# Kernel optimization log

Measured on AMD Instinct MI355X. Metric: run time of the kernel, lower is better.

## Reference

```python
import jax, jax.numpy as jnp
import numpy as np

B, N = 64, 4096          # trees per batch, leaves per complete binary tree
V, S = 21, 50            # amino-acid vocab, grammar-symbol vocab
E, H = 64, 128           # embed_dim, hidden_dim


def setup_inputs() -> dict:
    key = jax.random.key(0)
    ks = jax.random.split(key, 16)

    def lin_w(k, din, dout):
        return (jax.random.normal(k, (dout, din), jnp.float32) / np.sqrt(din)).astype(jnp.float32)

    tokens = jax.random.randint(ks[0], (B, N), 0, V, dtype=jnp.int32)
    symbols = jax.random.randint(ks[1], (B, N - 1), 0, S, dtype=jnp.int32)

    emb = jax.random.normal(ks[2], (V, E), jnp.float32) * 0.02
    emb = emb.at[0].set(0.0)  # padding_idx=0
    sym_emb = jax.random.normal(ks[3], (S, E), jnp.float32) * 0.02

    return {
        "tokens": tokens, "symbols": symbols,
        "emb": emb, "sym_emb": sym_emb,
        "Wp": lin_w(ks[4], E, H), "bp": jnp.zeros((H,), jnp.float32),
        "Wi": lin_w(ks[5], H, H), "bi": jnp.zeros((H,), jnp.float32),
        "Ui": lin_w(ks[6], H, H),
        "Wf": lin_w(ks[7], H, H), "bf": jnp.zeros((H,), jnp.float32),
        "Uf": lin_w(ks[8], H, H),
        "Wo": lin_w(ks[9], H, H), "bo": jnp.zeros((H,), jnp.float32),
        "Uo": lin_w(ks[10], H, H),
        "Wu": lin_w(ks[11], H, H), "bu": jnp.zeros((H,), jnp.float32),
        "Uu": lin_w(ks[12], H, H),
        "Wout": lin_w(ks[13], H, H), "bout": jnp.zeros((H,), jnp.float32),
    }


def _encode(tokens, symbols, emb, sym_emb, Wp, bp, Wi, bi, Ui, Wf, bf, Uf,
            Wo, bo, Uo, Wu, bu, Uu, Wout, bout):
    emb = emb.at[0].set(0.0)  # padding row contributes nothing (and gets no grad)

    # Leaf nodes: amino-acid embedding -> input_proj, no children.
    x = emb[tokens] @ Wp.T + bp                      # [B, N, H]
    i = jax.nn.sigmoid(x @ Wi.T + bi)
    o = jax.nn.sigmoid(x @ Wo.T + bo)
    u = jnp.tanh(x @ Wu.T + bu)
    c = i * u                                        # [B, N, H]
    h = o * jnp.tanh(c)

    # Bottom-up over levels of the complete binary tree (Child-Sum Tree-LSTM).
    off, n = 0, N
    while n > 1:
        m = n // 2
        xs = sym_emb[symbols[:, off:off + m]] @ Wp.T + bp   # [B, m, H]
        hl, hr = h[:, 0::2], h[:, 1::2]
        cl, cr = c[:, 0::2], c[:, 1::2]
        ht = hl + hr                                         # h_tilde = sum_j h_j
        gi = jax.nn.sigmoid(xs @ Wi.T + bi + ht @ Ui.T)
        go = jax.nn.sigmoid(xs @ Wo.T + bo + ht @ Uo.T)
        gu = jnp.tanh(xs @ Wu.T + bu + ht @ Uu.T)
        fx = xs @ Wf.T + bf
        fl = jax.nn.sigmoid(fx + hl @ Uf.T)                  # per-child forget gates
        fr = jax.nn.sigmoid(fx + hr @ Uf.T)
        c = gi * gu + fl * cl + fr * cr
        h = go * jnp.tanh(c)
        off += m
        n = m

    root_h = h[:, 0]                                         # [B, H]
    return root_h @ Wout.T + bout                            # output_proj


def reference(tokens, symbols, emb, sym_emb, Wp, bp, Wi, bi, Ui, Wf, bf, Uf,
              Wo, bo, Uo, Wu, bu, Uu, Wout, bout):
    return _encode(tokens, symbols, emb, sym_emb, Wp, bp, Wi, bi, Ui, Wf, bf,
                   Uf, Wo, bo, Uo, Wu, bu, Uu, Wout, bout)
```

## Files before the change

kernel.cpp:

```cpp
#include <hip/hip_runtime.h>
#include <hip/hip_bf16.h>

typedef __attribute__((ext_vector_type(8))) short short8;
typedef __attribute__((ext_vector_type(4))) float f32x4;

static constexpr int B_ = 64;
static constexpr int N_ = 4096;
static constexpr int V_ = 21;
static constexpr int S_ = 50;
static constexpr int E_ = 64;
static constexpr int H_ = 128;
static constexpr int NPAIR = V_ * V_;
static constexpr int NTAB = NPAIR * S_;

__device__ __forceinline__ float rcp_(float x) { return __builtin_amdgcn_rcpf(x); }
__device__ __forceinline__ float sigm(float x) { return rcp_(1.0f + __expf(-x)); }
__device__ __forceinline__ float tanh_(float x) {
  float a = fabsf(x);
  float e = __expf(-2.0f * a);
  float t = (1.0f - e) * rcp_(1.0f + e);
  return x < 0.0f ? -t : t;
}
__device__ __forceinline__ unsigned short f2bf(float f) {
  __hip_bfloat16 b = __float2bfloat16(f);
  return *reinterpret_cast<unsigned short*>(&b);
}
__device__ __forceinline__ float bf2f(unsigned short u) {
  return __uint_as_float(((unsigned int)u) << 16);
}

struct Gates { float cv, hv; };
__device__ __forceinline__ Gates gate_combine(const float* __restrict__ sx, int cc,
    float i_p, float o_p, float u_p, float fl_p, float fr_p, float cl, float cr) {
  float gi = sigm(sx[cc] + i_p);
  float go = sigm(sx[128 + cc] + o_p);
  float gu = tanh_(sx[256 + cc] + u_p);
  float fx = sx[384 + cc];
  float fl = sigm(fx + fl_p);
  float fr = sigm(fx + fr_p);
  float cv = fmaf(gi, gu, fmaf(fl, cl, fr * cr));
  Gates g; g.cv = cv; g.hv = go * tanh_(cv);
  return g;
}

__global__ void k_pre0(const float* __restrict__ Ui, const float* __restrict__ Uo,
                       const float* __restrict__ Uu, const float* __restrict__ Uf,
                       const float* __restrict__ Wi, const float* __restrict__ Wo,
                       const float* __restrict__ Wu, const float* __restrict__ Wf,
                       const float* __restrict__ Wp,
                       unsigned short* __restrict__ Wfrag, float* __restrict__ Wt,
                       float* __restrict__ Wxt, float* __restrict__ Wpt) {
  int blk = blockIdx.x, t = threadIdx.x;
  if (blk < 32) {
    int idx = blk * 256 + t;
    int L = idx & 63;
    int K = (idx >> 6) & 3;
    int T = idx >> 8;
    int n = 16 * T + (L & 15);
    int k0 = 32 * K + ((L >> 4) << 3);
    int g = n >> 7, o = n & 127;
    const float* U = (g == 0) ? Ui : (g == 1) ? Uo : (g == 2) ? Uu : Uf;
    unsigned short out[8];
    #pragma unroll
    for (int j = 0; j < 8; ++j) out[j] = f2bf(U[o * 128 + k0 + j]);
    *(int4*)(Wfrag + (size_t)idx * 8) = *(int4*)out;
  } else if (blk < 96) {
    bool isU = blk < 64;
    int base = (((blk & 31)) * 256 + t) * 8;
    int k = base >> 9;
    int col = base & 511;
    int gg = col >> 7, o0 = col & 127;
    const float* M;
    if (isU) M = (gg == 0) ? Ui : (gg == 1) ? Uo : (gg == 2) ? Uu : Uf;
    else     M = (gg == 0) ? Wi : (gg == 1) ? Wo : (gg == 2) ? Wu : Wf;
    float* D = isU ? Wt : Wxt;
    float v[8];
    #pragma unroll
    for (int j = 0; j < 8; ++j) v[j] = M[(o0 + j) * 128 + k];
    *(float4*)(D + base) = *(float4*)v;
    *(float4*)(D + base + 4) = *(float4*)(v + 4);
  } else {
    for (int i = t; i < E_ * H_; i += 256) {
      int e = i >> 7, o = i & 127;
      Wpt[i] = Wp[o * E_ + e];
    }
  }
}

__global__ void k_pre1(const float* __restrict__ emb, const float* __restrict__ sym_emb,
                       const float* __restrict__ Wpt, const float* __restrict__ Wxt,
                       const float* __restrict__ bp, const float* __restrict__ bi,
                       const float* __restrict__ bo, const float* __restrict__ bu,
                       const float* __restrict__ bfv,
                       unsigned short* __restrict__ leaf_h8, float* __restrict__ leaf_c,
                       float* __restrict__ symx) {
  int blk = blockIdx.x, t = threadIdx.x;
  __shared__ float x[128];
  if (blk < V_) {
    int v = blk;
    float acc = bp[t];
    if (v != 0) {
      for (int e = 0; e < E_; ++e) acc = fmaf(emb[v * E_ + e], Wpt[e * 128 + t], acc);
    }
    x[t] = acc;
    __syncthreads();
    float zi = bi[t], zo = bo[t], zu = bu[t];
    for (int k = 0; k < H_; ++k) {
      float xv = x[k];
      const float* wr = Wxt + k * 512;
      zi = fmaf(xv, wr[t], zi);
      zo = fmaf(xv, wr[128 + t], zo);
      zu = fmaf(xv, wr[256 + t], zu);
    }
    float gi = sigm(zi), go = sigm(zo), gu = tanh_(zu);
    float c = gi * gu;
    leaf_c[v * H_ + t] = c;
    leaf_h8[v * H_ + t] = f2bf(go * tanh_(c));
  } else {
    int s = blk - V_;
    float acc = bp[t];
    for (int e = 0; e < E_; ++e) acc = fmaf(sym_emb[s * E_ + e], Wpt[e * 128 + t], acc);
    x[t] = acc;
    __syncthreads();
    float zi = bi[t], zo = bo[t], zu = bu[t], zf = bfv[t];
    for (int k = 0; k < H_; ++k) {
      float xv = x[k];
      const float* wr = Wxt + k * 512;
      zi = fmaf(xv, wr[t], zi);
      zo = fmaf(xv, wr[128 + t], zo);
      zu = fmaf(xv, wr[256 + t], zu);
      zf = fmaf(xv, wr[384 + t], zf);
    }
    size_t base = (size_t)s * 4 * H_;
    symx[base + 0 * H_ + t] = zi;
    symx[base + 1 * H_ + t] = zo;
    symx[base + 2 * H_ + t] = zu;
    symx[base + 3 * H_ + t] = zf;
  }
}

__global__ void k_tabA(const unsigned short* __restrict__ leaf_h8, const float* __restrict__ Wt,
                       float* __restrict__ za) {
  int p = blockIdx.x, t = threadIdx.x;
  int tl = p / V_, tr = p % V_;
  __shared__ float hl[128], hr[128];
  hl[t] = bf2f(leaf_h8[tl * H_ + t]);
  hr[t] = bf2f(leaf_h8[tr * H_ + t]);
  __syncthreads();
  float zi = 0.f, zo = 0.f, zu = 0.f, pfl = 0.f, pfr = 0.f;
  for (int k = 0; k < H_; ++k) {
    float l = hl[k], r = hr[k], ht = l + r;
    const float* wr = Wt + k * 512;
    zi = fmaf(ht, wr[t], zi);
    zo = fmaf(ht, wr[128 + t], zo);
    zu = fmaf(ht, wr[256 + t], zu);
    float wf = wr[384 + t];
    pfl = fmaf(l, wf, pfl);
    pfr = fmaf(r, wf, pfr);
  }
  float* z = za + (size_t)p * 640;
  z[t] = zi; z[128 + t] = zo; z[256 + t] = zu; z[384 + t] = pfl; z[512 + t] = pfr;
}

__global__ void k_tabB(const float* __restrict__ za, const float* __restrict__ symx,
                       const float* __restrict__ leaf_c,
                       const int* __restrict__ tokens, const int* __restrict__ symbols,
                       unsigned short* __restrict__ tab_h8, float* __restrict__ tab_c,
                       int* __restrict__ idx1) {
  int blk = blockIdx.x, t = threadIdx.x;
  if (blk < NTAB / 2) {
    int row = blk * 2 + (t >> 7);
    int u = t & 127;
    int p = row / S_, s = row - p * S_;
    int tl = p / V_, tr = p - tl * V_;
    const float* z = za + (size_t)p * 640;
    const float* sx = symx + (size_t)s * 512;
    float gi = sigm(sx[u] + z[u]);
    float go = sigm(sx[128 + u] + z[128 + u]);
    float gu = tanh_(sx[256 + u] + z[256 + u]);
    float fx = sx[384 + u];
    float fl = sigm(fx + z[384 + u]);
    float fr = sigm(fx + z[512 + u]);
    float cv = fmaf(gi, gu, fmaf(fl, leaf_c[tl * H_ + u], fr * leaf_c[tr * H_ + u]));
    tab_c[(size_t)row * H_ + u] = cv;
    tab_h8[(size_t)row * H_ + u] = f2bf(go * tanh_(cv));
  } else {
    int g = (blk - NTAB / 2) * 256 + t;
    int b = g >> 11, j = g & 2047;
    idx1[g] = (tokens[b * N_ + 2 * j] * V_ + tokens[b * N_ + 2 * j + 1]) * S_ + symbols[b * (N_ - 1) + j];
  }
}

__global__ void __launch_bounds__(512, 4) k_lvl23(
    const unsigned short* __restrict__ Wfrag, const float* __restrict__ symx,
    const int* __restrict__ symbols, const int* __restrict__ idx1,
    const unsigned short* __restrict__ gh8, const float* __restrict__ gc,
    unsigned short* __restrict__ h_out8, float* __restrict__ c_out) {
  __shared__ __align__(16) unsigned short Ag[64][136];
  __shared__ __align__(16) unsigned short Bh[32][136];
  __shared__ float Bc[32][132];
  int t = threadIdx.x;
  int w = t >> 6, L = t & 63, q = L >> 4, cL = L & 15;
  int cc = 16 * w + cL;
  int g0 = blockIdx.x * 32;
  int b = g0 >> 10;
  int j2 = g0 & 1023;
  const int* sym_b = symbols + (size_t)b * (N_ - 1);
  const int* gix = idx1 + 2 * g0;

  #pragma unroll
  for (int i = 0; i < 2; ++i) {
    int fid = t + 512 * i;
    int row = fid >> 4, co = (fid & 15) * 8;
    *(int4*)&Ag[row][co] = *(const int4*)(gh8 + (size_t)gix[row] * H_ + co);
  }
  __syncthreads();

  const short8* wf = (const short8*)Wfrag;
  #pragma unroll
  for (int c = 0; c < 2; ++c) {
    f32x4 acc[2][4];
    #pragma unroll
    for (int r = 0; r < 2; ++r)
      #pragma unroll
      for (int g = 0; g < 4; ++g) acc[r][g] = (f32x4){0.f, 0.f, 0.f, 0.f};
    #pragma unroll
    for (int K = 0; K < 4; ++K) {
      short8 bfr[4];
      #pragma unroll
      for (int g = 0; g < 4; ++g) bfr[g] = wf[(size_t)((w + 8 * g) * 4 + K) * 64 + L];
      short8 a0 = *(const short8*)&Ag[32 * c + cL][K * 32 + q * 8];
      short8 a1 = *(const short8*)&Ag[32 * c + 16 + cL][K * 32 + q * 8];
      #pragma unroll
      for (int g = 0; g < 4; ++g) {
        acc[0][g] = __builtin_amdgcn_mfma_f32_16x16x32_bf16(a0, bfr[g], acc[0][g], 0, 0, 0);
        acc[1][g] = __builtin_amdgcn_mfma_f32_16x16x32_bf16(a1, bfr[g], acc[1][g], 0, 0, 0);
      }
    }
    #pragma unroll
    for (int r = 0; r < 2; ++r) {
      #pragma unroll
      for (int nd = 0; nd < 2; ++nd) {
        int n = 16 * c + 8 * r + 2 * q + nd;
        int s = sym_b[2048 + j2 + n];
        const float* sx = symx + (size_t)s * 512;
        float clv = gc[(size_t)gix[2 * n] * H_ + cc];
        float crv = gc[(size_t)gix[2 * n + 1] * H_ + cc];
        Gates gt = gate_combine(sx, cc,
            acc[r][0][2 * nd] + acc[r][0][2 * nd + 1],
            acc[r][1][2 * nd] + acc[r][1][2 * nd + 1],
            acc[r][2][2 * nd] + acc[r][2][2 * nd + 1],
            acc[r][3][2 * nd], acc[r][3][2 * nd + 1], clv, crv);
        Bc[n][cc] = gt.cv;
        Bh[n][cc] = f2bf(gt.hv);
      }
    }
  }
  __syncthreads();
  {
    f32x4 acc[2][4];
    #pragma unroll
    for (int r = 0; r < 2; ++r)
      #pragma unroll
      for (int g = 0; g < 4; ++g) acc[r][g] = (f32x4){0.f, 0.f, 0.f, 0.f};
    #pragma unroll
    for (int K = 0; K < 4; ++K) {
      short8 bfr[4];
      #pragma unroll
      for (int g = 0; g < 4; ++g) bfr[g] = wf[(size_t)((w + 8 * g) * 4 + K) * 64 + L];
      short8 a0 = *(const short8*)&Bh[cL][K * 32 + q * 8];
      short8 a1 = *(const short8*)&Bh[16 + cL][K * 32 + q * 8];
      #pragma unroll
      for (int g = 0; g < 4; ++g) {
        acc[0][g] = __builtin_amdgcn_mfma_f32_16x16x32_bf16(a0, bfr[g], acc[0][g], 0, 0, 0);
        acc[1][g] = __builtin_amdgcn_mfma_f32_16x16x32_bf16(a1, bfr[g], acc[1][g], 0, 0, 0);
      }
    }
    #pragma unroll
    for (int r = 0; r < 2; ++r) {
      #pragma unroll
      for (int nd = 0; nd < 2; ++nd) {
        int n = 8 * r + 2 * q + nd;
        int G3 = (g0 >> 1) + n;
        int s = sym_b[3072 + (j2 >> 1) + n];
        const float* sx = symx + (size_t)s * 512;
        Gates gt = gate_combine(sx, cc,
            acc[r][0][2 * nd] + acc[r][0][2 * nd + 1],
            acc[r][1][2 * nd] + acc[r][1][2 * nd + 1],
            acc[r][2][2 * nd] + acc[r][2][2 * nd + 1],
            acc[r][3][2 * nd], acc[r][3][2 * nd + 1],
            Bc[2 * n][cc], Bc[2 * n + 1][cc]);
        c_out[(size_t)G3 * H_ + cc] = gt.cv;
        h_out8[(size_t)G3 * H_ + cc] = f2bf(gt.hv);
      }
    }
  }
}

__global__ void __launch_bounds__(512, 4) k_lvl45(
    const unsigned short* __restrict__ Wfrag, const float* __restrict__ symx,
    const int* __restrict__ symbols,
    const unsigned short* __restrict__ in_h8, const float* __restrict__ in_c,
    unsigned short* __restrict__ h_out8, float* __restrict__ c_out) {
  __shared__ __align__(16) unsigned short Ag[64][136];
  __shared__ __align__(16) unsigned short Bh[32][136];
  __shared__ float Bc[32][132];
  int t = threadIdx.x;
  int w = t >> 6, L = t & 63, q = L >> 4, cL = L & 15;
  int cc = 16 * w + cL;
  int g0 = blockIdx.x * 32;
  int b = g0 >> 8;
  int j4 = g0 & 255;
  const int* sym_b = symbols + (size_t)b * (N_ - 1);

  #pragma unroll
  for (int i = 0; i < 2; ++i) {
    int fid = t + 512 * i;
    int row = fid >> 4, co = (fid & 15) * 8;
    *(int4*)&Ag[row][co] = *(const int4*)(in_h8 + (size_t)(2 * g0 + row) * H_ + co);
  }
  __syncthreads();

  const short8* wf = (const short8*)Wfrag;
  #pragma unroll
  for (int c = 0; c < 2; ++c) {
    f32x4 acc[2][4];
    #pragma unroll
    for (int r = 0; r < 2; ++r)
      #pragma unroll
      for (int g = 0; g < 4; ++g) acc[r][g] = (f32x4){0.f, 0.f, 0.f, 0.f};
    #pragma unroll
    for (int K = 0; K < 4; ++K) {
      short8 bfr[4];
      #pragma unroll
      for (int g = 0; g < 4; ++g) bfr[g] = wf[(size_t)((w + 8 * g) * 4 + K) * 64 + L];
      short8 a0 = *(const short8*)&Ag[32 * c + cL][K * 32 + q * 8];
      short8 a1 = *(const short8*)&Ag[32 * c + 16 + cL][K * 32 + q * 8];
      #pragma unroll
      for (int g = 0; g < 4; ++g) {
        acc[0][g] = __builtin_amdgcn_mfma_f32_16x16x32_bf16(a0, bfr[g], acc[0][g], 0, 0, 0);
        acc[1][g] = __builtin_amdgcn_mfma_f32_16x16x32_bf16(a1, bfr[g], acc[1][g], 0, 0, 0);
      }
    }
    #pragma unroll
    for (int r = 0; r < 2; ++r) {
      #pragma unroll
      for (int nd = 0; nd < 2; ++nd) {
        int n = 16 * c + 8 * r + 2 * q + nd;
        int g = g0 + n;
        int s = sym_b[3584 + j4 + n];
        const float* sx = symx + (size_t)s * 512;
        Gates gt = gate_combine(sx, cc,
            acc[r][0][2 * nd] + acc[r][0][2 * nd + 1],
            acc[r][1][2 * nd] + acc[r][1][2 * nd + 1],
            acc[r][2][2 * nd] + acc[r][2][2 * nd + 1],
            acc[r][3][2 * nd], acc[r][3][2 * nd + 1],
            in_c[(size_t)(2 * g) * H_ + cc], in_c[(size_t)(2 * g + 1) * H_ + cc]);
        Bc[n][cc] = gt.cv;
        Bh[n][cc] = f2bf(gt.hv);
      }
    }
  }
  __syncthreads();
  {
    f32x4 acc[2][4];
    #pragma unroll
    for (int r = 0; r < 2; ++r)
      #pragma unroll
      for (int g = 0; g < 4; ++g) acc[r][g] = (f32x4){0.f, 0.f, 0.f, 0.f};
    #pragma unroll
    for (int K = 0; K < 4; ++K) {
      short8 bfr[4];
      #pragma unroll
      for (int g = 0; g < 4; ++g) bfr[g] = wf[(size_t)((w + 8 * g) * 4 + K) * 64 + L];
      short8 a0 = *(const short8*)&Bh[cL][K * 32 + q * 8];
      short8 a1 = *(const short8*)&Bh[16 + cL][K * 32 + q * 8];
      #pragma unroll
      for (int g = 0; g < 4; ++g) {
        acc[0][g] = __builtin_amdgcn_mfma_f32_16x16x32_bf16(a0, bfr[g], acc[0][g], 0, 0, 0);
        acc[1][g] = __builtin_amdgcn_mfma_f32_16x16x32_bf16(a1, bfr[g], acc[1][g], 0, 0, 0);
      }
    }
    #pragma unroll
    for (int r = 0; r < 2; ++r) {
      #pragma unroll
      for (int nd = 0; nd < 2; ++nd) {
        int n = 8 * r + 2 * q + nd;
        int G5 = (g0 >> 1) + n;
        int s = sym_b[3840 + (j4 >> 1) + n];
        const float* sx = symx + (size_t)s * 512;
        Gates gt = gate_combine(sx, cc,
            acc[r][0][2 * nd] + acc[r][0][2 * nd + 1],
            acc[r][1][2 * nd] + acc[r][1][2 * nd + 1],
            acc[r][2][2 * nd] + acc[r][2][2 * nd + 1],
            acc[r][3][2 * nd], acc[r][3][2 * nd + 1],
            Bc[2 * n][cc], Bc[2 * n + 1][cc]);
        c_out[(size_t)G5 * H_ + cc] = gt.cv;
        h_out8[(size_t)G5 * H_ + cc] = f2bf(gt.hv);
      }
    }
  }
}

__global__ void __launch_bounds__(512, 2) k_lvl6(
    const unsigned short* __restrict__ Wfrag, const float* __restrict__ symx,
    const int* __restrict__ symbols,
    const unsigned short* __restrict__ h_prev8, const float* __restrict__ c_prev,
    unsigned short* __restrict__ h_out8, float* __restrict__ c_out) {
  __shared__ __align__(16) unsigned short Asm[32][136];
  int t = threadIdx.x;
  int w = t >> 6, L = t & 63, q = L >> 4, cL = L & 15;
  int g0 = blockIdx.x * 16;

  {
    int row = t >> 4, co = (t & 15) * 8;
    *(int4*)&Asm[row][co] = *(const int4*)(h_prev8 + (size_t)(2 * g0 + row) * H_ + co);
  }
  __syncthreads();

  f32x4 acc[2][4];
  #pragma unroll
  for (int r = 0; r < 2; ++r)
    #pragma unroll
    for (int g = 0; g < 4; ++g) acc[r][g] = (f32x4){0.f, 0.f, 0.f, 0.f};

  const short8* wf = (const short8*)Wfrag;
  #pragma unroll
  for (int K = 0; K < 4; ++K) {
    short8 bfr[4];
    #pragma unroll
    for (int g = 0; g < 4; ++g) bfr[g] = wf[(size_t)((w + 8 * g) * 4 + K) * 64 + L];
    short8 a0 = *(const short8*)&Asm[cL][K * 32 + q * 8];
    short8 a1 = *(const short8*)&Asm[16 + cL][K * 32 + q * 8];
    #pragma unroll
    for (int g = 0; g < 4; ++g) {
      acc[0][g] = __builtin_amdgcn_mfma_f32_16x16x32_bf16(a0, bfr[g], acc[0][g], 0, 0, 0);
      acc[1][g] = __builtin_amdgcn_mfma_f32_16x16x32_bf16(a1, bfr[g], acc[1][g], 0, 0, 0);
    }
  }

  int cc = 16 * w + cL;
  #pragma unroll
  for (int r = 0; r < 2; ++r) {
    #pragma unroll
    for (int nd = 0; nd < 2; ++nd) {
      int n = 8 * r + 2 * q + nd;
      int g = g0 + n;
      int bb = g >> 6, jj = g & 63;
      int s = symbols[bb * (N_ - 1) + 3968 + jj];
      const float* sx = symx + (size_t)s * 512;
      Gates gt = gate_combine(sx, cc,
          acc[r][0][2 * nd] + acc[r][0][2 * nd + 1],
          acc[r][1][2 * nd] + acc[r][1][2 * nd + 1],
          acc[r][2][2 * nd] + acc[r][2][2 * nd + 1],
          acc[r][3][2 * nd], acc[r][3][2 * nd + 1],
          c_prev[(size_t)(2 * g) * H_ + cc], c_prev[(size_t)(2 * g + 1) * H_ + cc]);
      c_out[(size_t)g * H_ + cc] = gt.cv;
      h_out8[(size_t)g * H_ + cc] = f2bf(gt.hv);
    }
  }
}

__global__ void __launch_bounds__(512, 1) k_deep(
    const unsigned short* __restrict__ Wfrag, const float* __restrict__ symx,
    const int* __restrict__ symbols,
    const unsigned short* __restrict__ in_h8, const float* __restrict__ in_c,
    float* __restrict__ out_root) {
  __shared__ __align__(16) unsigned short Asm[64][136];
  __shared__ float Csm0[64][128];
  __shared__ float Csm1[32][128];
  int t = threadIdx.x;
  int w = t >> 6, L = t & 63, q = L >> 4, cL = L & 15;
  int b = blockIdx.x;

  #pragma unroll
  for (int i = 0; i < 2; ++i) {
    int fid = t + 512 * i;
    int row = fid >> 4, co = (fid & 15) * 8;
    *(int4*)&Asm[row][co] = *(const int4*)(in_h8 + (size_t)(b * 64 + row) * H_ + co);
  }
  #pragma unroll
  for (int i = 0; i < 4; ++i) {
    int fid = t + 512 * i;
    int row = fid >> 5, c4 = (fid & 31) << 2;
    *(float4*)&Csm0[row][c4] = *(const float4*)(in_c + (size_t)(b * 64 + row) * H_ + c4);
  }
  __syncthreads();

  const short8* wf = (const short8*)Wfrag;
  int cc = 16 * w + cL;
  int R = 64;
  #pragma unroll
  for (int lev = 0; lev < 6; ++lev) {
    const int l = 7 + lev;
    const int nodes = R >> 1;
    const int jb = b * (N_ - 1) + (N_ - (N_ >> (l - 1)));
    const int nchunk = (R + 31) >> 5;
    for (int c = 0; c < nchunk; ++c) {
      f32x4 acc[2][4];
      #pragma unroll
      for (int r = 0; r < 2; ++r)
        #pragma unroll
        for (int g = 0; g < 4; ++g) acc[r][g] = (f32x4){0.f, 0.f, 0.f, 0.f};
      #pragma unroll
      for (int K = 0; K < 4; ++K) {
        short8 bfr[4];
        #pragma unroll
        for (int g = 0; g < 4; ++g) bfr[g] = wf[(size_t)((w + 8 * g) * 4 + K) * 64 + L];
        short8 a0 = *(const short8*)&Asm[32 * c + cL][K * 32 + q * 8];
        short8 a1 = *(const short8*)&Asm[32 * c + 16 + cL][K * 32 + q * 8];
        #pragma unroll
        for (int g = 0; g < 4; ++g) {
          acc[0][g] = __builtin_amdgcn_mfma_f32_16x16x32_bf16(a0, bfr[g], acc[0][g], 0, 0, 0);
          acc[1][g] = __builtin_amdgcn_mfma_f32_16x16x32_bf16(a1, bfr[g], acc[1][g], 0, 0, 0);
        }
      }
      __syncthreads();
      const float* crd = (l & 1) ? &Csm0[0][0] : &Csm1[0][0];
      float* cwr = (l & 1) ? &Csm1[0][0] : &Csm0[0][0];
      #pragma unroll
      for (int r = 0; r < 2; ++r) {
        #pragma unroll
        for (int nd = 0; nd < 2; ++nd) {
          int n = 16 * c + 8 * r + 2 * q + nd;
          if (n < nodes) {
            int s = symbols[jb + n];
            const float* sx = symx + (size_t)s * 512;
            Gates gt = gate_combine(sx, cc,
                acc[r][0][2 * nd] + acc[r][0][2 * nd + 1],
                acc[r][1][2 * nd] + acc[r][1][2 * nd + 1],
                acc[r][2][2 * nd] + acc[r][2][2 * nd + 1],
                acc[r][3][2 * nd], acc[r][3][2 * nd + 1],
                crd[(size_t)(2 * n) * 128 + cc], crd[(size_t)(2 * n + 1) * 128 + cc]);
            if (lev == 5) {
              out_root[(size_t)b * H_ + cc] = gt.hv;
            } else {
              cwr[(size_t)n * 128 + cc] = gt.cv;
              Asm[n][cc] = f2bf(gt.hv);
            }
          }
        }
      }
      __syncthreads();
    }
    R >>= 1;
  }
}

__global__ void k_out(const float* __restrict__ hroot, const float* __restrict__ Wout,
                      const float* __restrict__ bout, float* __restrict__ out) {
  int b = blockIdx.x, o = threadIdx.x;
  __shared__ float hr[128];
  hr[o] = hroot[(size_t)b * H_ + o];
  __syncthreads();
  float acc = bout[o];
  for (int k = 0; k < H_; ++k) acc = fmaf(hr[k], Wout[o * H_ + k], acc);
  out[(size_t)b * H_ + o] = acc;
}

extern "C" void kernel_launch(void* const* d_in, const int* in_sizes, int n_in,
                              void* d_out, int out_size, void* d_ws, size_t ws_size,
                              hipStream_t stream) {
  const int* tokens    = (const int*)d_in[0];
  const int* symbols   = (const int*)d_in[1];
  const float* emb     = (const float*)d_in[2];
  const float* sym_emb = (const float*)d_in[3];
  const float* Wp  = (const float*)d_in[4];
  const float* bp  = (const float*)d_in[5];
  const float* Wi  = (const float*)d_in[6];
  const float* bi  = (const float*)d_in[7];
  const float* Ui  = (const float*)d_in[8];
  const float* Wf  = (const float*)d_in[9];
  const float* bf  = (const float*)d_in[10];
  const float* Uf  = (const float*)d_in[11];
  const float* Wo  = (const float*)d_in[12];
  const float* bo  = (const float*)d_in[13];
  const float* Uo  = (const float*)d_in[14];
  const float* Wu  = (const float*)d_in[15];
  const float* bu  = (const float*)d_in[16];
  const float* Uu  = (const float*)d_in[17];
  const float* Wout= (const float*)d_in[18];
  const float* bout= (const float*)d_in[19];

  char* ws = (char*)d_ws;
  unsigned short* Wfrag   = (unsigned short*)(ws);
  float*          Wt      = (float*)(ws + 131072);
  float*          Wxt     = (float*)(ws + 393216);
  float*          Wpt     = (float*)(ws + 655360);
  unsigned short* leaf_h8 = (unsigned short*)(ws + 688128);
  float*          leaf_c  = (float*)(ws + 693504);
  float*          symx    = (float*)(ws + 704256);
  float*          za      = (float*)(ws + 806656);
  unsigned short* tab_h8  = (unsigned short*)(ws + 1935616);
  float*          tab_c   = (float*)(ws + 7580416UL);
  int*            idx1    = (int*)(ws + 18870016UL);
  float*          hroot   = (float*)(ws + 19394304UL);
  unsigned short* L3h8    = (unsigned short*)(ws + 19427072UL);
  float*          L3c     = (float*)(ws + 27815680UL);
  unsigned short* L5h8    = (unsigned short*)(ws + 44592896UL);
  float*          L5c     = (float*)(ws + 46690048UL);
  unsigned short* L6h8    = (unsigned short*)(ws + 50884352UL);
  float*          L6c     = (float*)(ws + 51932928UL);

  k_pre0<<<97, 256, 0, stream>>>(Ui, Uo, Uu, Uf, Wi, Wo, Wu, Wf, Wp,
                                 Wfrag, Wt, Wxt, Wpt);
  k_pre1<<<V_ + S_, 128, 0, stream>>>(emb, sym_emb, Wpt, Wxt,
                                      bp, bi, bo, bu, bf, leaf_h8, leaf_c, symx);
  k_tabA<<<NPAIR, 128, 0, stream>>>(leaf_h8, Wt, za);
  k_tabB<<<NTAB / 2 + 512, 256, 0, stream>>>(za, symx, leaf_c, tokens, symbols,
                                             tab_h8, tab_c, idx1);
  k_lvl23<<<2048, 512, 0, stream>>>(Wfrag, symx, symbols, idx1, tab_h8, tab_c, L3h8, L3c);
  k_lvl45<<<512, 512, 0, stream>>>(Wfrag, symx, symbols, L3h8, L3c, L5h8, L5c);
  k_lvl6<<<256, 512, 0, stream>>>(Wfrag, symx, symbols, L5h8, L5c, L6h8, L6c);
  k_deep<<<B_, 512, 0, stream>>>(Wfrag, symx, symbols, L6h8, L6c, hroot);
  k_out<<<B_, 128, 0, stream>>>(hroot, Wout, bout, (float*)d_out);
}
```

Before: 236.7 us.

## Interleave symx gates, prefetch child state, double-buffer deep levels, fuse output projection

Stores the per-symbol gate projections interleaved so each thread fetches its four gate values with one float4 load. Child cell states and symbol indices are loaded before the MFMA loops so their latency overlaps the matrix work. The deep kernel ping-pongs between two h/c buffers, dropping one barrier per chunk, and folds the output projection into its tail, removing the separate k_out launch. Launch bounds rise to 6 waves per SIMD, which caps registers and may cause spills.

```diff
diff --git a/kernel.cpp b/kernel.cpp
--- a/kernel.cpp
+++ b/kernel.cpp
@@ -30,14 +30,13 @@
 }
 
 struct Gates { float cv, hv; };
-__device__ __forceinline__ Gates gate_combine(const float* __restrict__ sx, int cc,
+__device__ __forceinline__ Gates gate_combine(float4 sx,
     float i_p, float o_p, float u_p, float fl_p, float fr_p, float cl, float cr) {
-  float gi = sigm(sx[cc] + i_p);
-  float go = sigm(sx[128 + cc] + o_p);
-  float gu = tanh_(sx[256 + cc] + u_p);
-  float fx = sx[384 + cc];
-  float fl = sigm(fx + fl_p);
-  float fr = sigm(fx + fr_p);
+  float gi = sigm(sx.x + i_p);
+  float go = sigm(sx.y + o_p);
+  float gu = tanh_(sx.z + u_p);
+  float fl = sigm(sx.w + fl_p);
+  float fr = sigm(sx.w + fr_p);
   float cv = fmaf(gi, gu, fmaf(fl, cl, fr * cr));
   Gates g; g.cv = cv; g.hv = go * tanh_(cv);
   return g;
@@ -47,9 +46,10 @@
                        const float* __restrict__ Uu, const float* __restrict__ Uf,
                        const float* __restrict__ Wi, const float* __restrict__ Wo,
                        const float* __restrict__ Wu, const float* __restrict__ Wf,
-                       const float* __restrict__ Wp,
+                       const float* __restrict__ Wp, const float* __restrict__ Wout,
                        unsigned short* __restrict__ Wfrag, float* __restrict__ Wt,
-                       float* __restrict__ Wxt, float* __restrict__ Wpt) {
+                       float* __restrict__ Wxt, float* __restrict__ Wpt,
+                       float* __restrict__ Woutt) {
   int blk = blockIdx.x, t = threadIdx.x;
   if (blk < 32) {
     int idx = blk * 256 + t;
@@ -79,10 +79,15 @@
     for (int j = 0; j < 8; ++j) v[j] = M[(o0 + j) * 128 + k];
     *(float4*)(D + base) = *(float4*)v;
     *(float4*)(D + base + 4) = *(float4*)(v + 4);
-  } else {
+  } else if (blk == 96) {
     for (int i = t; i < E_ * H_; i += 256) {
       int e = i >> 7, o = i & 127;
       Wpt[i] = Wp[o * E_ + e];
+    }
+  } else {
+    for (int i = t; i < H_ * H_; i += 256) {
+      int k = i >> 7, o = i & 127;
+      Woutt[i] = Wout[o * H_ + k];
     }
   }
 }
@@ -131,11 +136,8 @@
       zu = fmaf(xv, wr[256 + t], zu);
       zf = fmaf(xv, wr[384 + t], zf);
     }
-    size_t base = (size_t)s * 4 * H_;
-    symx[base + 0 * H_ + t] = zi;
-    symx[base + 1 * H_ + t] = zo;
-    symx[base + 2 * H_ + t] = zu;
-    symx[base + 3 * H_ + t] = zf;
+    float4 v4 = make_float4(zi, zo, zu, zf);
+    *(float4*)(symx + (size_t)s * 512 + t * 4) = v4;
   }
 }
 
@@ -174,16 +176,11 @@
     int p = row / S_, s = row - p * S_;
     int tl = p / V_, tr = p - tl * V_;
     const float* z = za + (size_t)p * 640;
-    const float* sx = symx + (size_t)s * 512;
-    float gi = sigm(sx[u] + z[u]);
-    float go = sigm(sx[128 + u] + z[128 + u]);
-    float gu = tanh_(sx[256 + u] + z[256 + u]);
-    float fx = sx[384 + u];
-    float fl = sigm(fx + z[384 + u]);
-    float fr = sigm(fx + z[512 + u]);
-    float cv = fmaf(gi, gu, fmaf(fl, leaf_c[tl * H_ + u], fr * leaf_c[tr * H_ + u]));
-    tab_c[(size_t)row * H_ + u] = cv;
-    tab_h8[(size_t)row * H_ + u] = f2bf(go * tanh_(cv));
+    float4 sx = *(const float4*)(symx + (size_t)s * 512 + u * 4);
+    Gates gt = gate_combine(sx, z[u], z[128 + u], z[256 + u], z[384 + u], z[512 + u],
+                            leaf_c[tl * H_ + u], leaf_c[tr * H_ + u]);
+    tab_c[(size_t)row * H_ + u] = gt.cv;
+    tab_h8[(size_t)row * H_ + u] = f2bf(gt.hv);
   } else {
     int g = (blk - NTAB / 2) * 256 + t;
     int b = g >> 11, j = g & 2047;
@@ -191,7 +188,7 @@
   }
 }
 
-__global__ void __launch_bounds__(512, 4) k_lvl23(
+__global__ void __launch_bounds__(512, 6) k_lvl23(
     const unsigned short* __restrict__ Wfrag, const float* __restrict__ symx,
     const int* __restrict__ symbols, const int* __restrict__ idx1,
     const unsigned short* __restrict__ gh8, const float* __restrict__ gc,
@@ -219,6 +216,15 @@
   const short8* wf = (const short8*)Wfrag;
   #pragma unroll
   for (int c = 0; c < 2; ++c) {
+    float clp[4], crp[4];
+    int spre[4];
+    #pragma unroll
+    for (int it = 0; it < 4; ++it) {
+      int n = 16 * c + 8 * (it >> 1) + 2 * q + (it & 1);
+      clp[it] = gc[(size_t)gix[2 * n] * H_ + cc];
+      crp[it] = gc[(size_t)gix[2 * n + 1] * H_ + cc];
+      spre[it] = sym_b[2048 + j2 + n];
+    }
     f32x4 acc[2][4];
     #pragma unroll
     for (int r = 0; r < 2; ++r)
@@ -241,16 +247,14 @@
     for (int r = 0; r < 2; ++r) {
       #pragma unroll
       for (int nd = 0; nd < 2; ++nd) {
+        int it = r * 2 + nd;
         int n = 16 * c + 8 * r + 2 * q + nd;
-        int s = sym_b[2048 + j2 + n];
-        const float* sx = symx + (size_t)s * 512;
-        float clv = gc[(size_t)gix[2 * n] * H_ + cc];
-        float crv = gc[(size_t)gix[2 * n + 1] * H_ + cc];
-        Gates gt = gate_combine(sx, cc,
+        float4 sx = *(const float4*)(symx + (size_t)spre[it] * 512 + cc * 4);
+        Gates gt = gate_combine(sx,
             acc[r][0][2 * nd] + acc[r][0][2 * nd + 1],
             acc[r][1][2 * nd] + acc[r][1][2 * nd + 1],
             acc[r][2][2 * nd] + acc[r][2][2 * nd + 1],
-            acc[r][3][2 * nd], acc[r][3][2 * nd + 1], clv, crv);
+            acc[r][3][2 * nd], acc[r][3][2 * nd + 1], clp[it], crp[it]);
         Bc[n][cc] = gt.cv;
         Bh[n][cc] = f2bf(gt.hv);
       }
@@ -258,6 +262,12 @@
   }
   __syncthreads();
   {
+    int spre[4];
+    #pragma unroll
+    for (int it = 0; it < 4; ++it) {
+      int n = 8 * (it >> 1) + 2 * q + (it & 1);
+      spre[it] = sym_b[3072 + (j2 >> 1) + n];
+    }
     f32x4 acc[2][4];
     #pragma unroll
     for (int r = 0; r < 2; ++r)
@@ -280,11 +290,11 @@
     for (int r = 0; r < 2; ++r) {
       #pragma unroll
       for (int nd = 0; nd < 2; ++nd) {
+        int it = r * 2 + nd;
         int n = 8 * r + 2 * q + nd;
         int G3 = (g0 >> 1) + n;
-        int s = sym_b[3072 + (j2 >> 1) + n];
-        const float* sx = symx + (size_t)s * 512;
-        Gates gt = gate_combine(sx, cc,
+        float4 sx = *(const float4*)(symx + (size_t)spre[it] * 512 + cc * 4);
+        Gates gt = gate_combine(sx,
             acc[r][0][2 * nd] + acc[r][0][2 * nd + 1],
             acc[r][1][2 * nd] + acc[r][1][2 * nd + 1],
             acc[r][2][2 * nd] + acc[r][2][2 * nd + 1],
@@ -297,7 +307,7 @@
   }
 }
 
-__global__ void __launch_bounds__(512, 4) k_lvl45(
+__global__ void __launch_bounds__(512, 6) k_lvl45(
     const unsigned short* __restrict__ Wfrag, const float* __restrict__ symx,
     const int* __restrict__ symbols,
     const unsigned short* __restrict__ in_h8, const float* __restrict__ in_c,
@@ -324,6 +334,16 @@
   const short8* wf = (const short8*)Wfrag;
   #pragma unroll
   for (int c = 0; c < 2; ++c) {
+    float clp[4], crp[4];
+    int spre[4];
+    #pragma unroll
+    for (int it = 0; it < 4; ++it) {
+      int n = 16 * c + 8 * (it >> 1) + 2 * q + (it & 1);
+      int g = g0 + n;
+      clp[it] = in_c[(size_t)(2 * g) * H_ + cc];
+      crp[it] = in_c[(size_t)(2 * g + 1) * H_ + cc];
+      spre[it] = sym_b[3584 + j4 + n];
+    }
     f32x4 acc[2][4];
     #pragma unroll
     for (int r = 0; r < 2; ++r)
@@ -346,16 +366,14 @@
     for (int r = 0; r < 2; ++r) {
       #pragma unroll
       for (int nd = 0; nd < 2; ++nd) {
+        int it = r * 2 + nd;
         int n = 16 * c + 8 * r + 2 * q + nd;
-        int g = g0 + n;
-        int s = sym_b[3584 + j4 + n];
-        const float* sx = symx + (size_t)s * 512;
-        Gates gt = gate_combine(sx, cc,
+        float4 sx = *(const float4*)(symx + (size_t)spre[it] * 512 + cc * 4);
+        Gates gt = gate_combine(sx,
             acc[r][0][2 * nd] + acc[r][0][2 * nd + 1],
             acc[r][1][2 * nd] + acc[r][1][2 * nd + 1],
             acc[r][2][2 * nd] + acc[r][2][2 * nd + 1],
-            acc[r][3][2 * nd], acc[r][3][2 * nd + 1],
-            in_c[(size_t)(2 * g) * H_ + cc], in_c[(size_t)(2 * g + 1) * H_ + cc]);
+            acc[r][3][2 * nd], acc[r][3][2 * nd + 1], clp[it], crp[it]);
         Bc[n][cc] = gt.cv;
         Bh[n][cc] = f2bf(gt.hv);
       }
@@ -363,6 +381,12 @@
   }
   __syncthreads();
   {
+    int spre[4];
+    #pragma unroll
+    for (int it = 0; it < 4; ++it) {
+      int n = 8 * (it >> 1) + 2 * q + (it & 1);
+      spre[it] = sym_b[3840 + (j4 >> 1) + n];
+    }
     f32x4 acc[2][4];
     #pragma unroll
     for (int r = 0; r < 2; ++r)
@@ -385,11 +409,11 @@
     for (int r = 0; r < 2; ++r) {
       #pragma unroll
       for (int nd = 0; nd < 2; ++nd) {
+        int it = r * 2 + nd;
         int n = 8 * r + 2 * q + nd;
         int G5 = (g0 >> 1) + n;
-        int s = sym_b[3840 + (j4 >> 1) + n];
-        const float* sx = symx + (size_t)s * 512;
-        Gates gt = gate_combine(sx, cc,
+        float4 sx = *(const float4*)(symx + (size_t)spre[it] * 512 + cc * 4);
+        Gates gt = gate_combine(sx,
             acc[r][0][2 * nd] + acc[r][0][2 * nd + 1],
             acc[r][1][2 * nd] + acc[r][1][2 * nd + 1],
             acc[r][2][2 * nd] + acc[r][2][2 * nd + 1],
@@ -410,8 +434,20 @@
   __shared__ __align__(16) unsigned short Asm[32][136];
   int t = threadIdx.x;
   int w = t >> 6, L = t & 63, q = L >> 4, cL = L & 15;
+  int cc = 16 * w + cL;
   int g0 = blockIdx.x * 16;
 
+  float clp[4], crp[4];
+  int spre[4];
+  #pragma unroll
+  for (int it = 0; it < 4; ++it) {
+    int n = 8 * (it >> 1) + 2 * q + (it & 1);
+    int g = g0 + n;
+    clp[it] = c_prev[(size_t)(2 * g) * H_ + cc];
+    crp[it] = c_prev[(size_t)(2 * g + 1) * H_ + cc];
+    int bb = g >> 6, jj = g & 63;
+    spre[it] = symbols[bb * (N_ - 1) + 3968 + jj];
+  }
   {
     int row = t >> 4, co = (t & 15) * 8;
     *(int4*)&Asm[row][co] = *(const int4*)(h_prev8 + (size_t)(2 * g0 + row) * H_ + co);
@@ -439,22 +475,19 @@
     }
   }
 
-  int cc = 16 * w + cL;
   #pragma unroll
   for (int r = 0; r < 2; ++r) {
     #pragma unroll
     for (int nd = 0; nd < 2; ++nd) {
+      int it = r * 2 + nd;
       int n = 8 * r + 2 * q + nd;
       int g = g0 + n;
-      int bb = g >> 6, jj = g & 63;
-      int s = symbols[bb * (N_ - 1) + 3968 + jj];
-      const float* sx = symx + (size_t)s * 512;
-      Gates gt = gate_combine(sx, cc,
+      float4 sx = *(const float4*)(symx + (size_t)spre[it] * 512 + cc * 4);
+      Gates gt = gate_combine(sx,
           acc[r][0][2 * nd] + acc[r][0][2 * nd + 1],
           acc[r][1][2 * nd] + acc[r][1][2 * nd + 1],
           acc[r][2][2 * nd] + acc[r][2][2 * nd + 1],
-          acc[r][3][2 * nd], acc[r][3][2 * nd + 1],
-          c_prev[(size_t)(2 * g) * H_ + cc], c_prev[(size_t)(2 * g + 1) * H_ + cc]);
+          acc[r][3][2 * nd], acc[r][3][2 * nd + 1], clp[it], crp[it]);
       c_out[(size_t)g * H_ + cc] = gt.cv;
       h_out8[(size_t)g * H_ + cc] = f2bf(gt.hv);
     }
@@ -465,30 +498,33 @@
     const unsigned short* __restrict__ Wfrag, const float* __restrict__ symx,
     const int* __restrict__ symbols,
     const unsigned short* __restrict__ in_h8, const float* __restrict__ in_c,
-    float* __restrict__ out_root) {
-  __shared__ __align__(16) unsigned short Asm[64][136];
-  __shared__ float Csm0[64][128];
-  __shared__ float Csm1[32][128];
+    const float* __restrict__ Woutt, const float* __restrict__ bout,
+    float* __restrict__ out) {
+  __shared__ __align__(16) unsigned short Ah0[64][136];
+  __shared__ __align__(16) unsigned short Ah1[32][136];
+  __shared__ float Cs0[64][128];
+  __shared__ float Cs1[32][128];
+  __shared__ float rootv[128];
   int t = threadIdx.x;
   int w = t >> 6, L = t & 63, q = L >> 4, cL = L & 15;
+  int cc = 16 * w + cL;
   int b = blockIdx.x;
 
   #pragma unroll
   for (int i = 0; i < 2; ++i) {
     int fid = t + 512 * i;
     int row = fid >> 4, co = (fid & 15) * 8;
-    *(int4*)&Asm[row][co] = *(const int4*)(in_h8 + (size_t)(b * 64 + row) * H_ + co);
+    *(int4*)&Ah0[row][co] = *(const int4*)(in_h8 + (size_t)(b * 64 + row) * H_ + co);
   }
   #pragma unroll
   for (int i = 0; i < 4; ++i) {
     int fid = t + 512 * i;
     int row = fid >> 5, c4 = (fid & 31) << 2;
-    *(float4*)&Csm0[row][c4] = *(const float4*)(in_c + (size_t)(b * 64 + row) * H_ + c4);
+    *(float4*)&Cs0[row][c4] = *(const float4*)(in_c + (size_t)(b * 64 + row) * H_ + c4);
   }
   __syncthreads();
 
   const short8* wf = (const short8*)Wfrag;
-  int cc = 16 * w + cL;
   int R = 64;
   #pragma unroll
   for (int lev = 0; lev < 6; ++lev) {
@@ -496,6 +532,15 @@
     const int nodes = R >> 1;
     const int jb = b * (N_ - 1) + (N_ - (N_ >> (l - 1)));
     const int nchunk = (R + 31) >> 5;
+    unsigned short (*Ard)[136] = (lev & 1) ? Ah1 : Ah0;
+    unsigned short (*Awr)[136] = (lev & 1) ? Ah0 : Ah1;
+    const float* crd = (lev & 1) ? &Cs1[0][0] : &Cs0[0][0];
+    float* cwr = (lev & 1) ? &Cs0[0][0] : &Cs1[0][0];
+    int spre[8];
+    for (int it = 0; it < 4 * nchunk; ++it) {
+      int n = 16 * (it >> 2) + 8 * ((it >> 1) & 1) + 2 * q + (it & 1);
+      spre[it] = (n < nodes) ? symbols[jb + n] : 0;
+    }
     for (int c = 0; c < nchunk; ++c) {
       f32x4 acc[2][4];
       #pragma unroll
@@ -507,55 +552,46 @@
         short8 bfr[4];
         #pragma unroll
         for (int g = 0; g < 4; ++g) bfr[g] = wf[(size_t)((w + 8 * g) * 4 + K) * 64 + L];
-        short8 a0 = *(const short8*)&Asm[32 * c + cL][K * 32 + q * 8];
-        short8 a1 = *(const short8*)&Asm[32 * c + 16 + cL][K * 32 + q * 8];
+        short8 a0 = *(const short8*)&Ard[32 * c + cL][K * 32 + q * 8];
+        short8 a1 = *(const short8*)&Ard[32 * c + 16 + cL][K * 32 + q * 8];
         #pragma unroll
         for (int g = 0; g < 4; ++g) {
           acc[0][g] = __builtin_amdgcn_mfma_f32_16x16x32_bf16(a0, bfr[g], acc[0][g], 0, 0, 0);
           acc[1][g] = __builtin_amdgcn_mfma_f32_16x16x32_bf16(a1, bfr[g], acc[1][g], 0, 0, 0);
         }
       }
-      __syncthreads();
-      const float* crd = (l & 1) ? &Csm0[0][0] : &Csm1[0][0];
-      float* cwr = (l & 1) ? &Csm1[0][0] : &Csm0[0][0];
       #pragma unroll
       for (int r = 0; r < 2; ++r) {
         #pragma unroll
         for (int nd = 0; nd < 2; ++nd) {
+          int it = c * 4 + r * 2 + nd;
           int n = 16 * c + 8 * r + 2 * q + nd;
           if (n < nodes) {
-            int s = symbols[jb + n];
-            const float* sx = symx + (size_t)s * 512;
-            Gates gt = gate_combine(sx, cc,
+            float4 sx = *(const float4*)(symx + (size_t)spre[it] * 512 + cc * 4);
+            Gates gt = gate_combine(sx,
                 acc[r][0][2 * nd] + acc[r][0][2 * nd + 1],
                 acc[r][1][2 * nd] + acc[r][1][2 * nd + 1],
                 acc[r][2][2 * nd] + acc[r][2][2 * nd + 1],
                 acc[r][3][2 * nd], acc[r][3][2 * nd + 1],
                 crd[(size_t)(2 * n) * 128 + cc], crd[(size_t)(2 * n + 1) * 128 + cc]);
             if (lev == 5) {
-              out_root[(size_t)b * H_ + cc] = gt.hv;
+              rootv[cc] = gt.hv;
             } else {
               cwr[(size_t)n * 128 + cc] = gt.cv;
-              Asm[n][cc] = f2bf(gt.hv);
+              Awr[n][cc] = f2bf(gt.hv);
             }
           }
         }
       }
-      __syncthreads();
-    }
+    }
+    __syncthreads();
     R >>= 1;
   }
-}
-
-__global__ void k_out(const float* __restrict__ hroot, const float* __restrict__ Wout,
-                      const float* __restrict__ bout, float* __restrict__ out) {
-  int b = blockIdx.x, o = threadIdx.x;
-  __shared__ float hr[128];
-  hr[o] = hroot[(size_t)b * H_ + o];
-  __syncthreads();
-  float acc = bout[o];
-  for (int k = 0; k < H_; ++k) acc = fmaf(hr[k], Wout[o * H_ + k], acc);
-  out[(size_t)b * H_ + o] = acc;
+  if (t < 128) {
+    float acc = bout[t];
+    for (int k = 0; k < H_; ++k) acc = fmaf(rootv[k], Woutt[k * 128 + t], acc);
+    out[(size_t)b * H_ + t] = acc;
+  }
 }
 
 extern "C" void kernel_launch(void* const* d_in, const int* in_sizes, int n_in,
@@ -587,23 +623,23 @@
   float*          Wt      = (float*)(ws + 131072);
   float*          Wxt     = (float*)(ws + 393216);
   float*          Wpt     = (float*)(ws + 655360);
-  unsigned short* leaf_h8 = (unsigned short*)(ws + 688128);
-  float*          leaf_c  = (float*)(ws + 693504);
-  float*          symx    = (float*)(ws + 704256);
-  float*          za      = (float*)(ws + 806656);
-  unsigned short* tab_h8  = (unsigned short*)(ws + 1935616);
-  float*          tab_c   = (float*)(ws + 7580416UL);
-  int*            idx1    = (int*)(ws + 18870016UL);
-  float*          hroot   = (float*)(ws + 19394304UL);
-  unsigned short* L3h8    = (unsigned short*)(ws + 19427072UL);
-  float*          L3c     = (float*)(ws + 27815680UL);
-  unsigned short* L5h8    = (unsigned short*)(ws + 44592896UL);
-  float*          L5c     = (float*)(ws + 46690048UL);
-  unsigned short* L6h8    = (unsigned short*)(ws + 50884352UL);
-  float*          L6c     = (float*)(ws + 51932928UL);
-
-  k_pre0<<<97, 256, 0, stream>>>(Ui, Uo, Uu, Uf, Wi, Wo, Wu, Wf, Wp,
-                                 Wfrag, Wt, Wxt, Wpt);
+  float*          Woutt   = (float*)(ws + 688128);
+  unsigned short* leaf_h8 = (unsigned short*)(ws + 753664);
+  float*          leaf_c  = (float*)(ws + 759040);
+  float*          symx    = (float*)(ws + 769792);
+  float*          za      = (float*)(ws + 872192);
+  unsigned short* tab_h8  = (unsigned short*)(ws + 2001152UL);
+  float*          tab_c   = (float*)(ws + 7645952UL);
+  int*            idx1    = (int*)(ws + 18935552UL);
+  unsigned short* L3h8    = (unsigned short*)(ws + 19459840UL);
+  float*          L3c     = (float*)(ws + 27848448UL);
+  unsigned short* L5h8    = (unsigned short*)(ws + 44625664UL);
+  float*          L5c     = (float*)(ws + 46722816UL);
+  unsigned short* L6h8    = (unsigned short*)(ws + 50917120UL);
+  float*          L6c     = (float*)(ws + 51965696UL);
+
+  k_pre0<<<98, 256, 0, stream>>>(Ui, Uo, Uu, Uf, Wi, Wo, Wu, Wf, Wp, Wout,
+                                 Wfrag, Wt, Wxt, Wpt, Woutt);
   k_pre1<<<V_ + S_, 128, 0, stream>>>(emb, sym_emb, Wpt, Wxt,
                                       bp, bi, bo, bu, bf, leaf_h8, leaf_c, symx);
   k_tabA<<<NPAIR, 128, 0, stream>>>(leaf_h8, Wt, za);
@@ -612,6 +648,6 @@
   k_lvl23<<<2048, 512, 0, stream>>>(Wfrag, symx, symbols, idx1, tab_h8, tab_c, L3h8, L3c);
   k_lvl45<<<512, 512, 0, stream>>>(Wfrag, symx, symbols, L3h8, L3c, L5h8, L5c);
   k_lvl6<<<256, 512, 0, stream>>>(Wfrag, symx, symbols, L5h8, L5c, L6h8, L6c);
-  k_deep<<<B_, 512, 0, stream>>>(Wfrag, symx, symbols, L6h8, L6c, hroot);
-  k_out<<<B_, 128, 0, stream>>>(hroot, Wout, bout, (float*)d_out);
-}
+  k_deep<<<B_, 512, 0, stream>>>(Wfrag, symx, symbols, L6h8, L6c, Woutt, bout,
+                                 (float*)d_out);
+}
```

New measurement: 240.5 us. Within noise of the previous version (+1.6%).
